# Kernel optimization log

Measured on AMD Instinct MI355X. Metric: run time of the kernel, lower is better.

## Reference

```python
import jax, jax.numpy as jnp
import numpy as np

N_NODES = 20000
N_EDGES = 480000
NUM_BATCH = 8     # B = batch_id.max()+1 (static)
NUM_GLOBAL = 3    # virtual_frame_num default
NUM_RBF = 16
EPS = 1e-20


def make_frames(n, ca, c):
    """OpenFold Rigid.make_transform_from_reference. Returns (R [N,3,3], t [N,3])."""
    nl = n - ca
    cl = c - ca
    cx, cy, cz = cl[:, 0], cl[:, 1], cl[:, 2]
    norm1 = jnp.sqrt(EPS + cx * cx + cy * cy)
    s1, c1 = -cy / norm1, cx / norm1
    norm2 = jnp.sqrt(EPS + cx * cx + cy * cy + cz * cz)
    s2, c2 = cz / norm2, jnp.sqrt(cx * cx + cy * cy) / norm2
    z = jnp.zeros_like(c1)
    o = jnp.ones_like(c1)
    R1 = jnp.stack([jnp.stack([c1, -s1, z], -1),
                    jnp.stack([s1, c1, z], -1),
                    jnp.stack([z, z, o], -1)], -2)          # rot about z
    R2 = jnp.stack([jnp.stack([c2, z, s2], -1),
                    jnp.stack([z, o, z], -1),
                    jnp.stack([-s2, z, c2], -1)], -2)       # rot about y
    Rc = jnp.einsum('nij,njk->nik', R2, R1)
    nr = jnp.einsum('nij,nj->ni', Rc, nl)
    ny, nz = nr[:, 1], nr[:, 2]
    norm3 = jnp.sqrt(EPS + ny * ny + nz * nz)
    sn, cn = -nz / norm3, ny / norm3
    Rn = jnp.stack([jnp.stack([o, z, z], -1),
                    jnp.stack([z, cn, -sn], -1),
                    jnp.stack([z, sn, cn], -1)], -2)        # rot about x
    R = jnp.einsum('nij,njk->nik', Rn, Rc).swapaxes(-1, -2)
    return R, ca


def rbf_encode(D):
    # D_min=0, D_max=20, 16 bins (matches rbf_func)
    mu = jnp.linspace(0.0, 20.0, NUM_RBF, dtype=D.dtype)
    sigma = 20.0 / NUM_RBF
    z = (D[..., None] - mu) / sigma
    return jnp.exp(-z * z)


def decouple(U):
    # safe norm: exact forward, NaN-free backward at U==0
    sq = jnp.sum(U * U, axis=-1, keepdims=True)
    norm = jnp.where(sq == 0, 0.0, jnp.sqrt(jnp.where(sq == 0, 1.0, sq)))
    direct = U / (norm + 1e-6)
    return jnp.concatenate([direct, rbf_encode(norm[..., 0])], axis=-1)


def int_embedding(d, num_embeddings):
    freq = jnp.exp(jnp.arange(0, num_embeddings, 2, dtype=jnp.float32)
                   * (-np.log(10000.0) / num_embeddings))
    ang = d[:, None].astype(jnp.float32) * freq[None, :]
    return jnp.concatenate([jnp.cos(ang), jnp.sin(ang)], -1)


def forward(X, edge_idx, batch_id, chain_encoding):
    N = X.shape[0]
    src, dst = edge_idx[0], edge_idx[1]
    R, t = make_frames(X[:, 0], X[:, 1], X[:, 2])
    # T_ts = T[dst].invert().compose(T[src]):  R_dst^T R_src,  R_dst^T (t_src - t_dst)
    R_ts = jnp.einsum('eji,ejk->eik', R[dst], R[src])
    t_ts = jnp.einsum('eji,ej->ei', R[dst], t[src] - t[dst])
    # --- node features ---
    diffX = jnp.diff(X.reshape(-1, 3), axis=0)
    diffX = jnp.concatenate([jnp.zeros((1, 3), X.dtype), diffX], 0).reshape(N, 4, 3)
    diffX_proj = jnp.einsum('nji,naj->nai', R, diffX)   # R^T @ diffX
    V = decouple(diffX_proj).reshape(N, -1)             # [N, 4*(3+16)=76]
    V = jnp.where(jnp.isnan(V), 0.0, V)
    # --- edge features ---
    atoms = jnp.concatenate([X[src], X[dst]], axis=1)   # [E,8,3]
    diffE = jnp.einsum('eji,eaj->eai', R[src], atoms - t[src][:, None, :])
    diffE = decouple(diffE).reshape(src.shape[0], -1)   # [E,152]
    pos_embed = int_embedding(src - dst, 16)            # [E,16]
    E_quant = R_ts.swapaxes(-1, -2).reshape(-1, 9)      # inverted rot mats
    E_trans = decouple(t_ts)                            # [E,19]
    Efeat = jnp.concatenate([diffE, E_quant, E_trans, pos_embed], -1)  # [E,196]
    # --- virtual (global) frames ---
    B, G = NUM_BATCH, NUM_GLOBAL
    g_src = jnp.concatenate([batch_id + N + k * B for k in range(G)])  # [G*N]
    g_dst = jnp.tile(jnp.arange(N, dtype=edge_idx.dtype), G)
    edge_idx_g = jnp.concatenate([jnp.stack([g_src, g_dst]),
                                  jnp.stack([g_dst, g_src])], axis=1)  # [2, 2*G*N]
    batch_id_g = jnp.tile(jnp.arange(B, dtype=batch_id.dtype), G)      # [G*B]
    h_V_g = jnp.tile(jnp.arange(G), B)                                 # [G*B]
    V_g = int_embedding(h_V_g, V.shape[-1]).astype(V.dtype)            # [G*B,76]
    n_ge = edge_idx_g.shape[1]
    E_g = jnp.zeros((n_ge, Efeat.shape[1]), Efeat.dtype)
    eye = jnp.eye(3, dtype=X.dtype)
    # --- merge local + global ---
    V_all = jnp.concatenate([V, V_g], 0)
    E_all = jnp.concatenate([Efeat, E_g], 0)
    R_all = jnp.concatenate([R, jnp.broadcast_to(eye, (G * B, 3, 3))], 0)
    t_all = jnp.concatenate([t, jnp.zeros((G * B, 3), X.dtype)], 0)
    Rts_all = jnp.concatenate([R_ts, jnp.broadcast_to(eye, (n_ge, 3, 3))], 0)
    tts_all = jnp.concatenate([t_ts, jnp.zeros((n_ge, 3), X.dtype)], 0)
    batch_all = jnp.concatenate([batch_id, batch_id_g])
    edge_all = jnp.concatenate([edge_idx, edge_idx_g], axis=1)
    chain_all = jnp.concatenate([chain_encoding, jnp.ones_like(batch_id_g) + 1000])
    return V_all, E_all, R_all, t_all, Rts_all, tts_all, batch_all, edge_all, chain_all


def setup_inputs() -> dict:
    key = jax.random.key(0)
    k1, k2, k3, k4 = jax.random.split(key, 4)
    X = jax.random.normal(k1, (N_NODES, 4, 3), dtype=jnp.float32)
    edge_idx = jax.random.randint(k2, (2, N_EDGES), 0, N_NODES, dtype=jnp.int32)
    batch_id = jnp.sort(jax.random.randint(k3, (N_NODES,), 0, NUM_BATCH, dtype=jnp.int32))
    chain_encoding = jax.random.randint(k4, (N_NODES,), 0, 10, dtype=jnp.int32)
    return {"X": X, "edge_idx": edge_idx, "batch_id": batch_id,
            "chain_encoding": chain_encoding}


def reference(X, edge_idx, batch_id, chain_encoding):
    return forward(X, edge_idx, batch_id, chain_encoding)
```

## Files before the change

### kernel.cpp

```cpp
#include <hip/hip_runtime.h>

#define NN 20000
#define NE 480000

#define OFF_V    0
#define OFF_E    1521824
#define OFF_R    119121824
#define OFF_T    119302040
#define OFF_RTS  119362112
#define OFF_TTS  124762112
#define OFF_BAT  126562112
#define OFF_EDG  126582136
#define OFF_CHN  127782136

#define REC 49

#define NB_EDGE 3750
#define NB_NODE 157
#define NB_FILL 49705
#define NB_TOTAL (NB_EDGE + NB_NODE + NB_FILL)

struct Frame { float m[3][3]; float t[3]; };

__device__ __forceinline__ void make_frame(const float a0[3], const float a1[3],
                                           const float a2[3], Frame& F){
  float nlx = a0[0]-a1[0], nly = a0[1]-a1[1], nlz = a0[2]-a1[2];
  float cx  = a2[0]-a1[0], cy  = a2[1]-a1[1], cz  = a2[2]-a1[2];
  float xy2 = cx*cx + cy*cy;
  float n1 = sqrtf(1e-20f + xy2);
  float s1 = -cy/n1, c1 = cx/n1;
  float n2 = sqrtf(1e-20f + xy2 + cz*cz);
  float s2 = cz/n2, c2 = sqrtf(xy2)/n2;
  float R00 = c2*c1, R01 = -c2*s1, R02 = s2;
  float R10 = s1,    R11 = c1,     R12 = 0.f;
  float R20 = -s2*c1,R21 = s2*s1,  R22 = c2;
  float nr1 = R10*nlx + R11*nly + R12*nlz;
  float nr2 = R20*nlx + R21*nly + R22*nlz;
  float n3 = sqrtf(1e-20f + nr1*nr1 + nr2*nr2);
  float sn = -nr2/n3, cn = nr1/n3;
  F.m[0][0]=R00;              F.m[0][1]=R01;              F.m[0][2]=R02;
  F.m[1][0]=cn*R10 - sn*R20;  F.m[1][1]=cn*R11 - sn*R21;  F.m[1][2]=cn*R12 - sn*R22;
  F.m[2][0]=sn*R10 + cn*R20;  F.m[2][1]=sn*R11 + cn*R21;  F.m[2][2]=sn*R12 + cn*R22;
  F.t[0]=a1[0]; F.t[1]=a1[1]; F.t[2]=a1[2];
}

__device__ __forceinline__ void group4(float ux, float uy, float uz, float* rec, int off){
  float sq = ux*ux + uy*uy + uz*uz;
  float nrm = (sq == 0.f) ? 0.f : sqrtf(sq);
  float inv = 1.0f / (nrm + 1e-6f);
  rec[off+0] = ux*inv; rec[off+1] = uy*inv; rec[off+2] = uz*inv; rec[off+3] = nrm;
}

__device__ __forceinline__ void decouple19(float ux, float uy, float uz, float* b){
  float sq = ux*ux + uy*uy + uz*uz;
  float nrm = (sq == 0.f) ? 0.f : sqrtf(sq);
  float inv = 1.0f / (nrm + 1e-6f);
  b[0] = ux*inv; b[1] = uy*inv; b[2] = uz*inv;
#pragma unroll
  for (int k = 0; k < 16; k++){
    float mu = (float)k * (20.0f/15.0f);
    float z = (nrm - mu) * 0.8f;
    b[3+k] = __expf(-z*z);
  }
}

__global__ __launch_bounds__(128) void mega_kernel(
    const float* __restrict__ X, const int* __restrict__ ei,
    const int* __restrict__ bat, const int* __restrict__ chn,
    float* __restrict__ out){
  __shared__ float lds[2*64*REC];
  const int blk = blockIdx.x;
  const int tid = threadIdx.x;

  if (blk < NB_EDGE){
    const int lane = tid & 63;
    const int wave = tid >> 6;
    const int e_my = blk*128 + tid;

    int src = ei[e_my], dst = ei[NE + e_my];
    const float* ps = X + (size_t)src*12;
    const float* pd = X + (size_t)dst*12;
    float as[4][3], ad[4][3];
#pragma unroll
    for (int i = 0; i < 12; i++){ as[i/3][i%3] = ps[i]; ad[i/3][i%3] = pd[i]; }
    Frame Fs, Fd;
    make_frame(as[0], as[1], as[2], Fs);
    make_frame(ad[0], ad[1], ad[2], Fd);

    float* rec = lds + (wave*64 + lane)*REC;

#pragma unroll
    for (int q = 0; q < 4; q++){
      float y0 = as[q][0]-Fs.t[0], y1 = as[q][1]-Fs.t[1], y2 = as[q][2]-Fs.t[2];
      group4(Fs.m[0][0]*y0 + Fs.m[0][1]*y1 + Fs.m[0][2]*y2,
             Fs.m[1][0]*y0 + Fs.m[1][1]*y1 + Fs.m[1][2]*y2,
             Fs.m[2][0]*y0 + Fs.m[2][1]*y1 + Fs.m[2][2]*y2, rec, 4*q);
    }
#pragma unroll
    for (int q = 0; q < 4; q++){
      float y0 = ad[q][0]-Fs.t[0], y1 = ad[q][1]-Fs.t[1], y2 = ad[q][2]-Fs.t[2];
      group4(Fs.m[0][0]*y0 + Fs.m[0][1]*y1 + Fs.m[0][2]*y2,
             Fs.m[1][0]*y0 + Fs.m[1][1]*y1 + Fs.m[1][2]*y2,
             Fs.m[2][0]*y0 + Fs.m[2][1]*y1 + Fs.m[2][2]*y2, rec, 16 + 4*q);
    }
#pragma unroll
    for (int i = 0; i < 3; i++)
#pragma unroll
      for (int k = 0; k < 3; k++)
        rec[36+3*i+k] = Fd.m[i][0]*Fs.m[k][0] + Fd.m[i][1]*Fs.m[k][1] + Fd.m[i][2]*Fs.m[k][2];
    {
      float d0 = Fs.t[0]-Fd.t[0], d1 = Fs.t[1]-Fd.t[1], d2 = Fs.t[2]-Fd.t[2];
      float t0 = Fd.m[0][0]*d0 + Fd.m[0][1]*d1 + Fd.m[0][2]*d2;
      float t1 = Fd.m[1][0]*d0 + Fd.m[1][1]*d1 + Fd.m[1][2]*d2;
      float t2 = Fd.m[2][0]*d0 + Fd.m[2][1]*d1 + Fd.m[2][2]*d2;
      rec[45] = t0; rec[46] = t1; rec[47] = t2;
      group4(t0, t1, t2, rec, 32);
    }
    rec[48] = (float)(src - dst);

    out[OFF_EDG + e_my]          = (float)src;
    out[OFF_EDG + 600000 + e_my] = (float)dst;


    const bool istrig = (lane >= 45 && lane <= 48);
    const bool iscos  = (lane < 47);
    int   offb[4];
    float msk[4], mu[4], frq[4];
#pragma unroll
    for (int c = 0; c < 4; c++){
      int j = 4*lane + c;
      int off = 0; float m = 0.f, rm = 0.f, fq = 0.f;
      if (j < 152){
        int jj = (j < 76) ? j : j - 76;
        int gq = ((j < 76) ? 0 : 4) + jj/19;
        int r  = jj - 19*(jj/19);
        if (r < 3) off = 4*gq + r;
        else { off = 4*gq + 3; m = 1.f; rm = (float)(r-3) * (20.0f/15.0f); }
      } else if (j < 161){
        int q = j - 152;
        off = 36 + 3*(q - 3*(q/3)) + q/3;
      } else if (j < 180){
        int r = j - 161;
        if (r < 3) off = 32 + r;
        else { off = 35; m = 1.f; rm = (float)(r-3) * (20.0f/15.0f); }
      } else if (j < 196){
        off = 48;
        int k = (j - 180) & 7;
        fq = exp2f(-(float)k * 1.6609640474436813f);
      } else {
        off = 0;
      }
      offb[c] = off; msk[c] = m; mu[c] = rm; frq[c] = fq;
    }

    const float* wlds = lds + wave*64*REC;
    const int wave_ebase = blk*128 + wave*64;
    float4* pstore = reinterpret_cast<float4*>(out + OFF_E + (size_t)wave_ebase*196) + lane;

#pragma unroll 2
    for (int e = 0; e < 64; e++){
      const float* r = wlds + e*REC;
      float v[4];
      if (istrig){
        float df = r[48];
#pragma unroll
        for (int c = 0; c < 4; c++){
          float ang = df * frq[c];
          v[c] = iscos ? __cosf(ang) : __sinf(ang);
        }
      } else {
#pragma unroll
        for (int c = 0; c < 4; c++){
          float x  = r[offb[c]];
          float z  = (x - mu[c]) * 0.8f;
          float rv = __expf(-z*z);
          v[c] = fmaf(msk[c], rv - x, x);
        }
      }
      if (lane < 49)
        *pstore = make_float4(v[0], v[1], v[2], v[3]);
      pstore += 49;
    }

#pragma unroll
    for (int k = 0; k < 9; k++){
      int f = k*64 + lane;
      int e = f/9, m = f - 9*e;
      out[OFF_RTS + (size_t)wave_ebase*9 + f] = wlds[e*REC + 36 + m];
    }
#pragma unroll
    for (int k = 0; k < 3; k++){
      int f = k*64 + lane;
      int e = f/3, m = f - 3*e;
      out[OFF_TTS + (size_t)wave_ebase*3 + f] = wlds[e*REC + 45 + m];
    }
    return;
  }

  if (blk < NB_EDGE + NB_NODE){
    int n = (blk - NB_EDGE)*128 + tid;
    if (n >= NN) return;
    const float* xp = X + (size_t)n*12;
    float a[4][3];
#pragma unroll
    for (int i = 0; i < 12; i++) a[i/3][i%3] = xp[i];
    Frame F; make_frame(a[0], a[1], a[2], F);

    float d[4][3];
    if (n > 0){ d[0][0]=a[0][0]-xp[-3]; d[0][1]=a[0][1]-xp[-2]; d[0][2]=a[0][2]-xp[-1]; }
    else      { d[0][0]=0.f; d[0][1]=0.f; d[0][2]=0.f; }
#pragma unroll
    for (int q = 1; q < 4; q++){
      d[q][0]=a[q][0]-a[q-1][0]; d[q][1]=a[q][1]-a[q-1][1]; d[q][2]=a[q][2]-a[q-1][2];
    }

    float buf[76];
#pragma unroll
    for (int q = 0; q < 4; q++){
      float vx = F.m[0][0]*d[q][0] + F.m[0][1]*d[q][1] + F.m[0][2]*d[q][2];
      float vy = F.m[1][0]*d[q][0] + F.m[1][1]*d[q][1] + F.m[1][2]*d[q][2];
      float vz = F.m[2][0]*d[q][0] + F.m[2][1]*d[q][1] + F.m[2][2]*d[q][2];
      decouple19(vx, vy, vz, buf + q*19);
    }
    float4* vrow = reinterpret_cast<float4*>(out + OFF_V + (size_t)n*76);
#pragma unroll
    for (int i = 0; i < 19; i++)
      vrow[i] = make_float4(buf[4*i], buf[4*i+1], buf[4*i+2], buf[4*i+3]);

    float* rr = out + OFF_R + (size_t)n*9;
#pragma unroll
    for (int i = 0; i < 3; i++)
#pragma unroll
      for (int j = 0; j < 3; j++) rr[3*i+j] = F.m[j][i];

    float* tr = out + OFF_T + (size_t)n*3;
#pragma unroll
    for (int i = 0; i < 3; i++) tr[i] = F.t[i];

    out[OFF_BAT + n] = (float)bat[n];
    out[OFF_CHN + n] = (float)chn[n];
    return;
  }

  int i = (blk - NB_EDGE - NB_NODE)*128 + tid;
  if (i < 5880000){
    uint4 z; z.x=0; z.y=0; z.z=0; z.w=0;
    reinterpret_cast<uint4*>(out + 95601824)[i] = z;
    return;
  }
  i -= 5880000;
  if (i < 90000){
    uint4 z; z.x=0; z.y=0; z.z=0; z.w=0;
    reinterpret_cast<uint4*>(out + 126202112)[i] = z;
    return;
  }
  i -= 90000;
  if (i < 270000){
    float v[4];
#pragma unroll
    for (int c = 0; c < 4; c++){
      int idx = 4*i + c;
      int r = idx % 9;
      v[c] = (r==0 || r==4 || r==8) ? 1.0f : 0.0f;
    }
    reinterpret_cast<float4*>(out + OFF_RTS + 4320000)[i] = make_float4(v[0],v[1],v[2],v[3]);
    return;
  }
  i -= 270000;
  if (i < 120000){
    int v0, v1;
    if (i < 60000){ int k = i/20000, m = i - 20000*k; v0 = bat[m] + 20000 + k*8; v1 = m; }
    else { int i2 = i - 60000; int k = i2/20000, m = i2 - 20000*k; v0 = m; v1 = bat[m] + 20000 + k*8; }
    out[OFF_EDG + 480000 + i]          = (float)v0;
    out[OFF_EDG + 600000 + 480000 + i] = (float)v1;
    return;
  }
  i -= 120000;
  if (i >= 2160) return;
  if (i < 1824){
    int r = i / 76, c = i % 76;
    float hv = (float)(r % 3);
    int j = (c < 38) ? c : c - 38;
    float fr = __expf(-(float)(2*j) * (9.210340371976184f/76.0f));
    float ang = hv * fr;
    out[OFF_V + 1520000 + i] = (c < 38) ? cosf(ang) : sinf(ang);
  } else if (i < 2040){
    int k = i - 1824; int r = k % 9;
    out[OFF_R + 180000 + k] = (r==0 || r==4 || r==8) ? 1.0f : 0.0f;
  } else if (i < 2112){
    out[OFF_T + 60000 + (i - 2040)] = 0.0f;
  } else if (i < 2136){
    int k = i - 2112;
    out[OFF_BAT + 20000 + k] = (float)(k % 8);
  } else {
    out[OFF_CHN + 20000 + (i - 2136)] = 1001.0f;
  }
}

extern "C" void kernel_launch(void* const* d_in, const int* in_sizes, int n_in,
                              void* d_out, int out_size, void* d_ws, size_t ws_size,
                              hipStream_t stream) {
  const float* X   = (const float*)d_in[0];
  const int* ei    = (const int*)d_in[1];
  const int* bat   = (const int*)d_in[2];
  const int* chn   = (const int*)d_in[3];
  float* out = (float*)d_out;

  mega_kernel<<<NB_TOTAL, 128, 0, stream>>>(X, ei, bat, chn, out);
}
```

Before: 118.7 us.

## Use nontemporal stores and move zero-fill regions to hipMemsetAsync

Large output writes (edge features, node features, rotations, identity fills) now use nontemporal vector stores so streaming output bypasses cache retention. The two bulk zero-fill regions are removed from the mega kernel and issued as separate hipMemsetAsync calls on the same stream, cutting the fill block count sharply. This adds two extra launches to the timed sequence in exchange for using the driver's memset path for roughly 95 MB of zeros.

```diff
diff --git a/kernel.cpp b/kernel.cpp
--- a/kernel.cpp
+++ b/kernel.cpp
@@ -17,10 +17,17 @@
 
 #define NB_EDGE 3750
 #define NB_NODE 157
-#define NB_FILL 49705
+#define NB_FILL 3064
 #define NB_TOTAL (NB_EDGE + NB_NODE + NB_FILL)
 
+typedef float floatx4 __attribute__((ext_vector_type(4)));
+
 struct Frame { float m[3][3]; float t[3]; };
+
+__device__ __forceinline__ void st_nt4(float* p, float a, float b, float c, float d){
+  floatx4 v; v.x = a; v.y = b; v.z = c; v.w = d;
+  __builtin_nontemporal_store(v, reinterpret_cast<floatx4*>(p));
+}
 
 __device__ __forceinline__ void make_frame(const float a0[3], const float a1[3],
                                            const float a2[3], Frame& F){
@@ -155,7 +162,7 @@
 
     const float* wlds = lds + wave*64*REC;
     const int wave_ebase = blk*128 + wave*64;
-    float4* pstore = reinterpret_cast<float4*>(out + OFF_E + (size_t)wave_ebase*196) + lane;
+    float* pstore = out + OFF_E + (size_t)wave_ebase*196 + 4*lane;
 
 #pragma unroll 2
     for (int e = 0; e < 64; e++){
@@ -178,21 +185,23 @@
         }
       }
       if (lane < 49)
-        *pstore = make_float4(v[0], v[1], v[2], v[3]);
-      pstore += 49;
+        st_nt4(pstore, v[0], v[1], v[2], v[3]);
+      pstore += 196;
     }
 
 #pragma unroll
     for (int k = 0; k < 9; k++){
       int f = k*64 + lane;
       int e = f/9, m = f - 9*e;
-      out[OFF_RTS + (size_t)wave_ebase*9 + f] = wlds[e*REC + 36 + m];
+      __builtin_nontemporal_store(wlds[e*REC + 36 + m],
+                                  out + OFF_RTS + (size_t)wave_ebase*9 + f);
     }
 #pragma unroll
     for (int k = 0; k < 3; k++){
       int f = k*64 + lane;
       int e = f/3, m = f - 3*e;
-      out[OFF_TTS + (size_t)wave_ebase*3 + f] = wlds[e*REC + 45 + m];
+      __builtin_nontemporal_store(wlds[e*REC + 45 + m],
+                                  out + OFF_TTS + (size_t)wave_ebase*3 + f);
     }
     return;
   }
@@ -222,10 +231,10 @@
       float vz = F.m[2][0]*d[q][0] + F.m[2][1]*d[q][1] + F.m[2][2]*d[q][2];
       decouple19(vx, vy, vz, buf + q*19);
     }
-    float4* vrow = reinterpret_cast<float4*>(out + OFF_V + (size_t)n*76);
+    float* vrow = out + OFF_V + (size_t)n*76;
 #pragma unroll
     for (int i = 0; i < 19; i++)
-      vrow[i] = make_float4(buf[4*i], buf[4*i+1], buf[4*i+2], buf[4*i+3]);
+      st_nt4(vrow + 4*i, buf[4*i], buf[4*i+1], buf[4*i+2], buf[4*i+3]);
 
     float* rr = out + OFF_R + (size_t)n*9;
 #pragma unroll
@@ -243,18 +252,6 @@
   }
 
   int i = (blk - NB_EDGE - NB_NODE)*128 + tid;
-  if (i < 5880000){
-    uint4 z; z.x=0; z.y=0; z.z=0; z.w=0;
-    reinterpret_cast<uint4*>(out + 95601824)[i] = z;
-    return;
-  }
-  i -= 5880000;
-  if (i < 90000){
-    uint4 z; z.x=0; z.y=0; z.z=0; z.w=0;
-    reinterpret_cast<uint4*>(out + 126202112)[i] = z;
-    return;
-  }
-  i -= 90000;
   if (i < 270000){
     float v[4];
 #pragma unroll
@@ -263,7 +260,7 @@
       int r = idx % 9;
       v[c] = (r==0 || r==4 || r==8) ? 1.0f : 0.0f;
     }
-    reinterpret_cast<float4*>(out + OFF_RTS + 4320000)[i] = make_float4(v[0],v[1],v[2],v[3]);
+    st_nt4(out + OFF_RTS + 4320000 + 4*(size_t)i, v[0], v[1], v[2], v[3]);
     return;
   }
   i -= 270000;
@@ -307,4 +304,6 @@
   float* out = (float*)d_out;
 
   mega_kernel<<<NB_TOTAL, 128, 0, stream>>>(X, ei, bat, chn, out);
-}
+  (void)hipMemsetAsync((void*)(out + 95601824), 0, 23520000ull*4, stream);
+  (void)hipMemsetAsync((void*)(out + 126202112), 0, 360000ull*4, stream);
+}
```

Result: slower. 150.4 us (+26.7%).
